# Kernel tuning notes

Hardware: AMD Instinct MI355X
Metric: run time of the kernel (lower is better)

The kernel has to match this reference:

```python
import jax, jax.numpy as jnp
import numpy as np

B, Din, T, G = 8, 512, 1024, 128
DM, H, L, FF = 512, 8, 2, 2048
MAX_PERIOD = 10000.0


def _ln(x, s, b, eps=1e-5):
    m = x.mean(-1, keepdims=True)
    v = ((x - m) ** 2).mean(-1, keepdims=True)
    return (x - m) * jax.lax.rsqrt(v + eps) * s + b


def _rope(x, pos):
    # x: (B,H,S,Dh), pos: (S,)
    dh = x.shape[-1]
    half = dh // 2
    freqs = 1.0 / (MAX_PERIOD ** (jnp.arange(half, dtype=jnp.float32) / half))
    ang = pos[:, None] * freqs[None, :]              # (S, half)
    cos, sin = jnp.cos(ang), jnp.sin(ang)
    x1, x2 = x[..., :half], x[..., half:]
    return jnp.concatenate([x1 * cos - x2 * sin, x1 * sin + x2 * cos], axis=-1)


def _transformer(x, W_in, b_in, ln1_s, ln1_b, Wq, Wk, Wv, Wo, ls1,
                 ln2_s, ln2_b, W1, b1, W2, b2, ls2, lnf_s, lnf_b, W_out, b_out):
    # x: (B, Din, S) conv layout -> (B, S, DM)
    h = jnp.einsum('bds,de->bse', x, W_in) + b_in
    Bx, S, E = h.shape
    dh = E // H
    pos = jnp.arange(S, dtype=jnp.float32)
    scale = 1.0 / jnp.sqrt(jnp.asarray(dh, h.dtype))
    for l in range(Wq.shape[0]):
        y = _ln(h, ln1_s[l], ln1_b[l])
        q = (y @ Wq[l]).reshape(Bx, S, H, dh).transpose(0, 2, 1, 3)
        k = (y @ Wk[l]).reshape(Bx, S, H, dh).transpose(0, 2, 1, 3)
        v = (y @ Wv[l]).reshape(Bx, S, H, dh).transpose(0, 2, 1, 3)
        q, k = _rope(q, pos), _rope(k, pos)
        att = jax.nn.softmax(jnp.einsum('bhqd,bhkd->bhqk', q, k) * scale, axis=-1)
        o = jnp.einsum('bhqk,bhkd->bhqd', att, v).transpose(0, 2, 1, 3).reshape(Bx, S, E)
        h = h + ls1[l] * (o @ Wo[l])
        y = _ln(h, ln2_s[l], ln2_b[l])
        h = h + ls2[l] * (jax.nn.gelu(y @ W1[l] + b1[l]) @ W2[l] + b2[l])
    h = _ln(h, lnf_s, lnf_b)
    return (h @ W_out + b_out).transpose(0, 2, 1)  # (B, Din, S)


def _forward(features, alignment_matrix, num_segments_per_item, params):
    Bx, D, Tt = features.shape
    Gx = alignment_matrix.shape[1]
    ar_t = jnp.arange(Tt, dtype=jnp.int32)
    ar_g = jnp.arange(Gx, dtype=jnp.int32)
    group_mask = ar_g[None, :] < num_segments_per_item[:, None]          # (B,G)
    group_last = (alignment_matrix * ar_t.astype(features.dtype)).max(axis=2).astype(jnp.int32)  # (B,G)
    valid_last = jnp.where(group_mask, group_last, -1)
    frame_lengths = valid_last.max(axis=1) + 1                            # (B,)
    frame_mask = ar_t[None, :] < frame_lengths[:, None]                   # (B,T)
    last_for_count = jnp.where(group_mask, group_last, Tt + 1)
    num_q_before = jnp.sum(last_for_count[:, :, None] < ar_t[None, None, :], axis=1).astype(jnp.int32)  # (B,T)
    frame_dest = ar_t[None, :] + num_q_before                             # (B,T)
    query_dest = group_last + ar_g[None, :] + 1                           # (B,G)
    # mean-pooled query init
    summed = jnp.einsum('bgt,bdt->bgd', alignment_matrix, features)
    counts = jnp.maximum(alignment_matrix.sum(axis=2), 1.0)
    queries = (summed / counts[..., None]).transpose(0, 2, 1)             # (B,D,G)
    source_seq = jnp.concatenate([features, queries], axis=2)             # (B,D,T+G)
    dest = jnp.concatenate([frame_dest, query_dest], axis=1)              # (B,T+G)
    smask = jnp.concatenate([frame_mask, group_mask], axis=1)
    dest_m = jnp.where(smask, dest, Tt + Gx)
    perm = jnp.argsort(dest_m, axis=1)                                    # (B,T+G)
    interleaved = jnp.take_along_axis(source_seq, perm[:, None, :], axis=2)
    tout = _transformer(interleaved, *params)                             # (B,D,T+G)
    inv_perm = jnp.argsort(perm, axis=1)
    qpos = inv_perm[:, Tt:]                                               # (B,G)
    agg = jnp.take_along_axis(tout, qpos[:, None, :], axis=2)             # (B,D,G)
    return jnp.where(group_mask[:, None, :], agg, 0.0)


def setup_inputs() -> dict:
    key = jax.random.key(0)
    ks = jax.random.split(key, 8)
    rng = np.random.default_rng(0)
    align = np.zeros((B, G, T), np.float32)
    num_seg = np.zeros((B,), np.int32)
    for b in range(B):
        n = int(rng.integers(G // 2, G + 1))
        cuts = np.sort(rng.choice(np.arange(1, T), n - 1, replace=False))
        gid = np.searchsorted(cuts, np.arange(T), side='right')
        align[b, gid, np.arange(T)] = 1.0
        num_seg[b] = n
    s = 0.02
    return {
        'features': jax.random.normal(ks[0], (B, Din, T), jnp.float32),
        'alignment_matrix': jnp.asarray(align),
        'num_segments_per_item': jnp.asarray(num_seg),
        'W_in': jax.random.normal(ks[1], (Din, DM), jnp.float32) * s,
        'b_in': jnp.zeros((DM,), jnp.float32),
        'ln1_s': jnp.ones((L, DM), jnp.float32), 'ln1_b': jnp.zeros((L, DM), jnp.float32),
        'Wq': jax.random.normal(ks[2], (L, DM, DM), jnp.float32) * s,
        'Wk': jax.random.normal(ks[3], (L, DM, DM), jnp.float32) * s,
        'Wv': jax.random.normal(ks[4], (L, DM, DM), jnp.float32) * s,
        'Wo': jax.random.normal(ks[5], (L, DM, DM), jnp.float32) * s,
        'ls1': 0.01 * jnp.ones((L, DM), jnp.float32),
        'ln2_s': jnp.ones((L, DM), jnp.float32), 'ln2_b': jnp.zeros((L, DM), jnp.float32),
        'W1': jax.random.normal(ks[6], (L, DM, FF), jnp.float32) * s,
        'b1': jnp.zeros((L, FF), jnp.float32),
        'W2': jax.random.normal(ks[7], (L, FF, DM), jnp.float32) * s,
        'b2': jnp.zeros((L, DM), jnp.float32),
        'ls2': 0.01 * jnp.ones((L, DM), jnp.float32),
        'lnf_s': jnp.ones((DM,), jnp.float32), 'lnf_b': jnp.zeros((DM,), jnp.float32),
        'W_out': jax.random.normal(jax.random.fold_in(key, 9), (DM, Din), jnp.float32) * s,
        'b_out': jnp.zeros((Din,), jnp.float32),
    }


def reference(features, alignment_matrix, num_segments_per_item, W_in, b_in, ln1_s, ln1_b,
              Wq, Wk, Wv, Wo, ls1, ln2_s, ln2_b, W1, b1, W2, b2, ls2, lnf_s, lnf_b, W_out, b_out):
    params = (W_in, b_in, ln1_s, ln1_b, Wq, Wk, Wv, Wo, ls1,
              ln2_s, ln2_b, W1, b1, W2, b2, ls2, lnf_s, lnf_b, W_out, b_out)
    return _forward(features, alignment_matrix, num_segments_per_item, params)
```

## Files before the change

### kernel.cpp

```cpp
#include <hip/hip_runtime.h>
#include <hip/hip_bf16.h>
#include <math.h>

#define NB   8
#define NT   1024
#define NG   128
#define NS   1152
#define NDIN 512
#define NDM  512
#define NH   8
#define NDH  64
#define NFF  2048
#define NL   2

typedef __attribute__((ext_vector_type(4))) float  floatx4;
typedef __attribute__((ext_vector_type(8))) short  shortx8;

__device__ __forceinline__ float gelu_f(float x) {
    float u = 1.5957691216057308f * (x + 0.044715f * x * x * x);
    return x / (1.0f + __expf(-u));
}

__device__ __forceinline__ void gload_lds16(const void* g, void* l) {
    __builtin_amdgcn_global_load_lds((const __attribute__((address_space(1))) unsigned int*)g,
                                     (__attribute__((address_space(3))) unsigned int*)l, 16, 0, 0);
}

__device__ __forceinline__ short f2bfs(float x) {
    __hip_bfloat16 h = __float2bfloat16(x);
    return *(short*)&h;
}
__device__ __forceinline__ unsigned pack_bf2(float a, float b) {
    __hip_bfloat16 x = __float2bfloat16(a), y = __float2bfloat16(b);
    return ((unsigned)(*(unsigned short*)&y) << 16) | (*(unsigned short*)&x);
}

__global__ __launch_bounds__(256) void ropetab_k(float2* __restrict__ tab)
{
    const int idx = blockIdx.x * 256 + threadIdx.x;
    if (idx >= NS * 32) return;
    const int s = idx >> 5, i = idx & 31;
    const float fr = __expf(-(float)i * 0.28782313662425576f);
    const float ang = (float)s * fr;
    tab[idx] = make_float2(cosf(ang), sinf(ang));
}

__global__ __launch_bounds__(256) void pool_k(const float* __restrict__ align,
        const float* __restrict__ features, int* __restrict__ glast,
        float* __restrict__ queries)
{
    __shared__ float redf[256];
    __shared__ int   redi[256];
    __shared__ float aw[NT];
    const int bg = blockIdx.x;
    const int b = bg >> 7;
    const int tid = threadIdx.x;
    const float* arow = align + (size_t)bg * NT;
    float cnt = 0.f, last = 0.f;
    int tmin = NT;
    for (int t = tid; t < NT; t += 256) {
        float a = arow[t];
        cnt += a;
        last = fmaxf(last, a * (float)t);
        if (a > 0.f) tmin = min(tmin, t);
    }
    redf[tid] = cnt; __syncthreads();
    for (int s = 128; s > 0; s >>= 1) { if (tid < s) redf[tid] += redf[tid + s]; __syncthreads(); }
    float c = redf[0]; __syncthreads();
    redf[tid] = last; __syncthreads();
    for (int s = 128; s > 0; s >>= 1) { if (tid < s) redf[tid] = fmaxf(redf[tid], redf[tid + s]); __syncthreads(); }
    float l = redf[0];
    redi[tid] = tmin; __syncthreads();
    for (int s = 128; s > 0; s >>= 1) { if (tid < s) redi[tid] = min(redi[tid], redi[tid + s]); __syncthreads(); }
    const int t0 = redi[0];
    const int t1 = (int)l;
    if (tid == 0) glast[bg] = t1;
    __syncthreads();
    for (int t = t0 + tid; t <= t1; t += 256) aw[t - t0] = arow[t];
    __syncthreads();
    const float invc = 1.0f / fmaxf(c, 1.0f);
    for (int d = tid; d < NDIN; d += 256) {
        const float* frow = features + ((size_t)b * NDIN + d) * NT;
        float s = 0.f;
        for (int t = t0; t <= t1; ++t) s += aw[t - t0] * frow[t];
        queries[(size_t)bg * NDIN + d] = s * invc;
    }
}

__global__ __launch_bounds__(256) void rank_k(const int* __restrict__ glast,
        const int* __restrict__ nsegp, int* __restrict__ perm, int* __restrict__ qpos)
{
    __shared__ int dm[NS];
    __shared__ int gl[NG];
    const int b = blockIdx.y;
    const int tid = threadIdx.x;
    const int j = blockIdx.x * 256 + tid;
    if (tid < NG) gl[tid] = glast[b * NG + tid];
    const int ns = nsegp[b];
    __syncthreads();
    for (int jj = tid; jj < NS; jj += 256) {
        int d;
        if (jj < NT) {
            int t = jj, nq = 0, flen = 0;
            for (int g = 0; g < ns; ++g) {
                flen = max(flen, gl[g] + 1);
                nq += (gl[g] < t) ? 1 : 0;
            }
            d = (t < flen) ? (t + nq) : NS;
        } else {
            int g = jj - NT;
            d = (g < ns) ? (gl[g] + g + 1) : NS;
        }
        dm[jj] = d;
    }
    __syncthreads();
    if (j < NS) {
        const int my = dm[j];
        int r = 0;
        for (int t = 0; t < NS; ++t) {
            int v2 = dm[t];
            r += (v2 < my || (v2 == my && t < j)) ? 1 : 0;
        }
        perm[b * NS + r] = j;
        if (j >= NT) qpos[b * NG + (j - NT)] = r;
    }
}

__global__ __launch_bounds__(256) void buildx_k(const float* __restrict__ features,
        const float* __restrict__ queries, const int* __restrict__ perm,
        __hip_bfloat16* __restrict__ X)
{
    const int idx = blockIdx.x * 256 + threadIdx.x;
    if (idx >= NB * NS * NDIN) return;
    const int d = idx & (NDIN - 1);
    const int p = (idx >> 9) % NS;
    const int b = idx / (NS * NDIN);
    const int j = perm[b * NS + p];
    float v = (j < NT) ? features[((size_t)b * NDIN + d) * NT + j]
                       : queries[((size_t)(b * NG + (j - NT))) * NDIN + d];
    X[idx] = __float2bfloat16(v);
}

__device__ __forceinline__ void wtile(const float* __restrict__ src,
        __hip_bfloat16* __restrict__ dst, int K, int N, int i, int tid, short tile[32][33])
{
    const int gx = N / 32;
    const int n0 = (i % gx) * 32;
    const int k0 = (i / gx) * 32;
    {
        const int r = tid >> 3, c4 = (tid & 7) * 4;
        float4 v = *(const float4*)&src[(size_t)(k0 + r) * N + n0 + c4];
        tile[c4 + 0][r] = f2bfs(v.x);
        tile[c4 + 1][r] = f2bfs(v.y);
        tile[c4 + 2][r] = f2bfs(v.z);
        tile[c4 + 3][r] = f2bfs(v.w);
    }
    __syncthreads();
    {
        const int r = tid >> 3, c4 = (tid & 7) * 4;
        short* dp = (short*)dst + (size_t)(n0 + r) * K + k0 + c4;
        short4 v;
        v.x = tile[r][c4 + 0]; v.y = tile[r][c4 + 1];
        v.z = tile[r][c4 + 2]; v.w = tile[r][c4 + 3];
        *(short4*)dp = v;
    }
}

__global__ __launch_bounds__(256) void wtransall_k(
        const float* W_in, const float* Wq, const float* Wk, const float* Wv,
        const float* Wo, const float* W1, const float* W2, const float* W_out,
        __hip_bfloat16* w_inT, __hip_bfloat16* wqkvT0, __hip_bfloat16* wqkvT1,
        __hip_bfloat16* woT0, __hip_bfloat16* woT1,
        __hip_bfloat16* w1T0, __hip_bfloat16* w1T1,
        __hip_bfloat16* w2T0, __hip_bfloat16* w2T1, __hip_bfloat16* woutT)
{
    __shared__ short tile[32][33];
    const int tid = threadIdx.x;
    const int i = blockIdx.x;
    const float* src; __hip_bfloat16* dst; int K, N, ti;
    if (i < 256) { src = W_in; dst = w_inT; K = 512; N = 512; ti = i; }
    else if (i < 6400) {
        int r = i - 256;
        const int l = r / 3072; r -= l * 3072;
        const size_t o5 = (size_t)l * 262144, o2 = (size_t)l * 1048576;
        if (r < 256)       { src = Wq + o5; dst = (l ? wqkvT1 : wqkvT0);          K = 512;  N = 512;  ti = r; }
        else if (r < 512)  { src = Wk + o5; dst = (l ? wqkvT1 : wqkvT0) + 262144; K = 512;  N = 512;  ti = r - 256; }
        else if (r < 768)  { src = Wv + o5; dst = (l ? wqkvT1 : wqkvT0) + 524288; K = 512;  N = 512;  ti = r - 512; }
        else if (r < 1024) { src = Wo + o5; dst = (l ? woT1 : woT0);              K = 512;  N = 512;  ti = r - 768; }
        else if (r < 2048) { src = W1 + o2; dst = (l ? w1T1 : w1T0);              K = 512;  N = 2048; ti = r - 1024; }
        else               { src = W2 + o2; dst = (l ? w2T1 : w2T0);              K = 2048; N = 512;  ti = r - 2048; }
    }
    else { src = W_out; dst = woutT; K = 512; N = 512; ti = i - 6400; }
    wtile(src, dst, K, N, ti, tid, tile);
}

__global__ __launch_bounds__(256) void bgemmw1_k(const __hip_bfloat16* __restrict__ A,
        const __hip_bfloat16* __restrict__ Bt, __hip_bfloat16* __restrict__ Cout,
        const float* __restrict__ bias, int M, int N, int K)
{
    __shared__ __align__(16) short SM[4][128 * 32];
    short* As0 = SM[0]; short* As1 = SM[1];
    short* Bs0 = SM[2]; short* Bs1 = SM[3];
    const int tid = threadIdx.x;
    const int wave = tid >> 6, lane = tid & 63;
    const int quad = lane >> 4, l16 = lane & 15;
    const int wm = wave >> 1, wn = wave & 1;
    const size_t bm = (size_t)blockIdx.y * 128, bn = (size_t)blockIdx.x * 128;
    const int sw = (l16 >> 1) & 3;
    const short* Ag = (const short*)A;
    const short* Bg = (const short*)Bt;
    const int lrow = lane >> 2;
    const int lchunk = (lane & 3) ^ ((lane >> 3) & 3);

    floatx4 acc[4][4];
#pragma unroll
    for (int i = 0; i < 4; ++i)
#pragma unroll
        for (int j = 0; j < 4; ++j) acc[i][j] = (floatx4){0.f, 0.f, 0.f, 0.f};

    for (int k0 = 0; k0 < K; k0 += 64) {
        __syncthreads();
#pragma unroll
        for (int c = 0; c < 2; ++c) {
            const int r0 = (c * 4 + wave) * 16;
            const size_t ra = (bm + r0 + lrow) * (size_t)K + k0 + lchunk * 8;
            const size_t rb = (bn + r0 + lrow) * (size_t)K + k0 + lchunk * 8;
            gload_lds16(Ag + ra,      &As0[r0 * 32]);
            gload_lds16(Ag + ra + 32, &As1[r0 * 32]);
            gload_lds16(Bg + rb,      &Bs0[r0 * 32]);
            gload_lds16(Bg + rb + 32, &Bs1[r0 * 32]);
        }
        __syncthreads();
#pragma unroll
        for (int h = 0; h < 2; ++h) {
            const short* Asrc = h ? As1 : As0;
            const short* Bsrc = h ? Bs1 : Bs0;
            shortx8 af[4], bf[4];
#pragma unroll
            for (int t = 0; t < 4; ++t) {
                af[t] = *(const shortx8*)&Asrc[(wm * 64 + t * 16 + l16) * 32 + ((quad ^ sw) * 8)];
                bf[t] = *(const shortx8*)&Bsrc[(wn * 64 + t * 16 + l16) * 32 + ((quad ^ sw) * 8)];
            }
#pragma unroll
            for (int mt = 0; mt < 4; ++mt)
#pragma unroll
                for (int nt = 0; nt < 4; ++nt)
                    acc[mt][nt] = __builtin_amdgcn_mfma_f32_16x16x32_bf16(af[mt], bf[nt], acc[mt][nt], 0, 0, 0);
        }
    }
    __syncthreads();
    const size_t mbase = bm + wm * 64;
    const size_t nbase = bn + wn * 64;
    short* ep = &SM[wave][0];
#pragma unroll
    for (int nt = 0; nt < 4; ++nt) {
        const size_t n = nbase + nt * 16 + l16;
        const float bz = bias[n];
        const int col = nt * 16 + l16;
#pragma unroll
        for (int mt = 0; mt < 4; ++mt)
#pragma unroll
            for (int r = 0; r < 4; ++r) {
                const int rl = mt * 16 + quad * 4 + r;
                float e = gelu_f(acc[mt][nt][r] + bz);
                ep[rl * 64 + (((col >> 3) ^ (rl & 7)) * 8) + (col & 7)] = f2bfs(e);
            }
    }
    __asm__ __volatile__("" ::: "memory");
#pragma unroll
    for (int c2 = 0; c2 < 8; ++c2) {
        const int rl = c2 * 8 + (lane >> 3);
        const int cc = lane & 7;
        shortx8 v = *(const shortx8*)&ep[rl * 64 + ((cc ^ (rl & 7)) * 8)];
        *(shortx8*)((short*)Cout + (mbase + rl) * N + nbase + cc * 8) = v;
    }
}

__global__ __launch_bounds__(256) void bgemmqkv_k(const __hip_bfloat16* __restrict__ A,
        const __hip_bfloat16* __restrict__ Bt, __hip_bfloat16* __restrict__ qh,
        __hip_bfloat16* __restrict__ kh, __hip_bfloat16* __restrict__ vT,
        const float2* __restrict__ tab)
{
    __shared__ __align__(16) short SM[4][128 * 32];
    short* As0 = SM[0]; short* As1 = SM[1];
    short* Bs0 = SM[2]; short* Bs1 = SM[3];
    const int tid = threadIdx.x;
    const int wave = tid >> 6, lane = tid & 63;
    const int quad = lane >> 4, l16 = lane & 15;
    const int wm = wave >> 1, wn = wave & 1;
    const size_t bm = (size_t)blockIdx.y * 128, bn = (size_t)blockIdx.x * 128;
    const int sw = (l16 >> 1) & 3;
    const int K = 512;
    const short* Ag = (const short*)A;
    const short* Bg = (const short*)Bt;
    const int lrow = lane >> 2;
    const int lchunk = (lane & 3) ^ ((lane >> 3) & 3);

    floatx4 acc[4][4];
#pragma unroll
    for (int i = 0; i < 4; ++i)
#pragma unroll
        for (int j = 0; j < 4; ++j) acc[i][j] = (floatx4){0.f, 0.f, 0.f, 0.f};

    for (int k0 = 0; k0 < K; k0 += 64) {
        __syncthreads();
#pragma unroll
        for (int c = 0; c < 2; ++c) {
            const int r0 = (c * 4 + wave) * 16;
            const size_t ra = (bm + r0 + lrow) * (size_t)K + k0 + lchunk * 8;
            const size_t rb = (bn + r0 + lrow) * (size_t)K + k0 + lchunk * 8;
            gload_lds16(Ag + ra,      &As0[r0 * 32]);
            gload_lds16(Ag + ra + 32, &As1[r0 * 32]);
            gload_lds16(Bg + rb,      &Bs0[r0 * 32]);
            gload_lds16(Bg + rb + 32, &Bs1[r0 * 32]);
        }
        __syncthreads();
#pragma unroll
        for (int h = 0; h < 2; ++h) {
            const short* Asrc = h ? As1 : As0;
            const short* Bsrc = h ? Bs1 : Bs0;
            shortx8 af[4], bf[4];
#pragma unroll
            for (int t = 0; t < 4; ++t) {
                af[t] = *(const shortx8*)&Asrc[(wm * 64 + t * 16 + l16) * 32 + ((quad ^ sw) * 8)];
                bf[t] = *(const shortx8*)&Bsrc[(wn * 64 + t * 16 + l16) * 32 + ((quad ^ sw) * 8)];
            }
#pragma unroll
            for (int mt = 0; mt < 4; ++mt)
#pragma unroll
                for (int nt = 0; nt < 4; ++nt)
                    acc[mt][nt] = __builtin_amdgcn_mfma_f32_16x16x32_bf16(af[mt], bf[nt], acc[mt][nt], 0, 0, 0);
        }
    }
    __syncthreads();
    short* ep = &SM[wave][0];
    const int bidx = (int)(bm / NS);
    const int sbase = (int)(bm - (size_t)bidx * NS) + wm * 64;
    const int region = (int)(bn >> 9);
    if (region < 2) {
        const float qsc = region ? 1.0f : 0.18033688011112043f;
        const int h = (int)((((int)bn & 511) + wn * 64) >> 6);
#pragma unroll
        for (int nt = 0; nt < 2; ++nt) {
            const int d1 = nt * 16 + l16, d2 = d1 + 32;
            const float2* tp = tab + d1;
#pragma unroll
            for (int mt = 0; mt < 4; ++mt)
#pragma unroll
                for (int r = 0; r < 4; ++r) {
                    const int sl = mt * 16 + quad * 4 + r;
                    const int s = sbase + sl;
                    float x1 = acc[mt][nt][r], x2 = acc[mt][nt + 2][r];
                    float2 cs = tp[s * 32];
                    ep[sl * 64 + (((d1 >> 3) ^ (sl & 7)) * 8) + (d1 & 7)] = f2bfs(qsc * (x1 * cs.x - x2 * cs.y));
                    ep[sl * 64 + (((d2 >> 3) ^ (sl & 7)) * 8) + (d2 & 7)] = f2bfs(qsc * (x1 * cs.y + x2 * cs.x));
                }
        }
        __asm__ __volatile__("" ::: "memory");
        short* dst = (short*)(region ? kh : qh) + ((size_t)(bidx * NH + h)) * NS * NDH;
#pragma unroll
        for (int c2 = 0; c2 < 8; ++c2) {
            const int sl = c2 * 8 + (lane >> 3);
            const int cc = lane & 7;
            shortx8 v = *(const shortx8*)&ep[sl * 64 + ((cc ^ (sl & 7)) * 8)];
            *(shortx8*)(dst + (size_t)(sbase + sl) * NDH + cc * 8) = v;
        }
    } else {
        const int base = (int)(bn - 1024) + wn * 64;
        const int h = base >> 6;
#pragma unroll
        for (int nt = 0; nt < 4; ++nt) {
            const int dl = nt * 16 + l16;
#pragma unroll
            for (int mt = 0; mt < 4; ++mt)
#pragma unroll
                for (int r = 0; r < 4; ++r) {
                    const int sl = mt * 16 + quad * 4 + r;
                    ep[dl * 64 + (((sl >> 3) ^ (dl & 7)) * 8) + (sl & 7)] = f2bfs(acc[mt][nt][r]);
                }
        }
        __asm__ __volatile__("" ::: "memory");
        short* vp = (short*)vT + ((size_t)(bidx * NH + h)) * NDH * NS;
#pragma unroll
        for (int c2 = 0; c2 < 8; ++c2) {
            const int dl = c2 * 8 + (lane >> 3);
            const int cc = lane & 7;
            shortx8 v = *(const shortx8*)&ep[dl * 64 + ((cc ^ (dl & 7)) * 8)];
            *(shortx8*)(vp + (size_t)dl * NS + sbase + cc * 8) = v;
        }
    }
}

template <int EPI>
__global__ __launch_bounds__(256) void bgemm64_k(const __hip_bfloat16* __restrict__ A,
        const __hip_bfloat16* __restrict__ Bt, void* __restrict__ Cout,
        const float* __restrict__ bias, const float* __restrict__ ls,
        const float* __restrict__ res, const int* __restrict__ nsegp, int M, int N, int K)
{
    __shared__ __align__(16) short As0[64 * 32], As1[64 * 32];
    __shared__ __align__(16) short Bs0[128 * 32], Bs1[128 * 32];
    const int tid = threadIdx.x;
    const int wave = tid >> 6, lane = tid & 63;
    const int quad = lane >> 4, l16 = lane & 15;
    const int wm = wave >> 1, wn = wave & 1;
    const size_t bm = (size_t)blockIdx.y * 64, bn = (size_t)blockIdx.x * 128;
    const int sw = (l16 >> 1) & 3;
    const short* Ag = (const short*)A;
    const short* Bg = (const short*)Bt;
    const int lrow = lane >> 2;
    const int lchunk = (lane & 3) ^ ((lane >> 3) & 3);

    floatx4 acc[2][4];
#pragma unroll
    for (int i = 0; i < 2; ++i)
#pragma unroll
        for (int j = 0; j < 4; ++j) acc[i][j] = (floatx4){0.f, 0.f, 0.f, 0.f};

    for (int k0 = 0; k0 < K; k0 += 64) {
        __syncthreads();
        {
            const int rA = wave * 16;
            const size_t ra = (bm + rA + lrow) * (size_t)K + k0 + lchunk * 8;
            gload_lds16(Ag + ra,      &As0[rA * 32]);
            gload_lds16(Ag + ra + 32, &As1[rA * 32]);
            const int rB = wave * 32;
            const size_t rb0 = (bn + rB + lrow) * (size_t)K + k0 + lchunk * 8;
            const size_t rb1 = (bn + rB + 16 + lrow) * (size_t)K + k0 + lchunk * 8;
            gload_lds16(Bg + rb0,      &Bs0[rB * 32]);
            gload_lds16(Bg + rb1,      &Bs0[(rB + 16) * 32]);
            gload_lds16(Bg + rb0 + 32, &Bs1[rB * 32]);
            gload_lds16(Bg + rb1 + 32, &Bs1[(rB + 16) * 32]);
        }
        __syncthreads();
#pragma unroll
        for (int h = 0; h < 2; ++h) {
            const short* Asrc = h ? As1 : As0;
            const short* Bsrc = h ? Bs1 : Bs0;
            shortx8 af[2], bf[4];
#pragma unroll
            for (int t = 0; t < 2; ++t)
                af[t] = *(const shortx8*)&Asrc[(wm * 32 + t * 16 + l16) * 32 + ((quad ^ sw) * 8)];
#pragma unroll
            for (int t = 0; t < 4; ++t)
                bf[t] = *(const shortx8*)&Bsrc[(wn * 64 + t * 16 + l16) * 32 + ((quad ^ sw) * 8)];
#pragma unroll
            for (int mt = 0; mt < 2; ++mt)
#pragma unroll
                for (int nt = 0; nt < 4; ++nt)
                    acc[mt][nt] = __builtin_amdgcn_mfma_f32_16x16x32_bf16(af[mt], bf[nt], acc[mt][nt], 0, 0, 0);
        }
    }
    const size_t mbase = bm + wm * 32;
    const size_t nbase = bn + wn * 64;
#pragma unroll
    for (int nt = 0; nt < 4; ++nt) {
        const size_t n = nbase + nt * 16 + l16;
        const float bz = bias ? bias[n] : 0.f;
        const float lz = (EPI == 2) ? ls[n] : 0.f;
#pragma unroll
        for (int mt = 0; mt < 2; ++mt) {
#pragma unroll
            for (int r = 0; r < 4; ++r) {
                const size_t m = mbase + mt * 16 + quad * 4 + r;
                float e = acc[mt][nt][r] + bz;
                if (EPI == 4) {
                    const int b = (int)(m >> 7), g = (int)(m & 127);
                    float val = (g < nsegp[b]) ? e : 0.0f;
                    ((float*)Cout)[(size_t)b * (NDIN * NG) + n * NG + g] = val;
                } else {
                    const size_t off = m * N + n;
                    if (EPI == 2) e = res[off] + lz * e;
                    ((float*)Cout)[off] = e;
                }
            }
        }
    }
}

__global__ __launch_bounds__(256) void lnw_k(const float* __restrict__ in,
        __hip_bfloat16* __restrict__ out, const float* __restrict__ gam, const float* __restrict__ bet)
{
    const int r = blockIdx.x * 4 + (threadIdx.x >> 6);
    const int t = threadIdx.x & 63;
    const float4* xp = (const float4*)(in + (size_t)r * NDM);
    float4 a = xp[t * 2], b4 = xp[t * 2 + 1];
    float s = a.x + a.y + a.z + a.w + b4.x + b4.y + b4.z + b4.w;
#pragma unroll
    for (int o = 1; o < 64; o <<= 1) s += __shfl_xor(s, o);
    const float mean = s * (1.0f / NDM);
    float dx[8] = {a.x - mean, a.y - mean, a.z - mean, a.w - mean,
                   b4.x - mean, b4.y - mean, b4.z - mean, b4.w - mean};
    float v = 0.f;
#pragma unroll
    for (int i = 0; i < 8; ++i) v += dx[i] * dx[i];
#pragma unroll
    for (int o = 1; o < 64; o <<= 1) v += __shfl_xor(v, o);
    const float inv = rsqrtf(v * (1.0f / NDM) + 1e-5f);
    const float4* gp = (const float4*)gam;
    const float4* bp = (const float4*)bet;
    float4 g0 = gp[t * 2], g1 = gp[t * 2 + 1], q0 = bp[t * 2], q1 = bp[t * 2 + 1];
    shortx8 o8;
    o8[0] = f2bfs(dx[0] * inv * g0.x + q0.x);
    o8[1] = f2bfs(dx[1] * inv * g0.y + q0.y);
    o8[2] = f2bfs(dx[2] * inv * g0.z + q0.z);
    o8[3] = f2bfs(dx[3] * inv * g0.w + q0.w);
    o8[4] = f2bfs(dx[4] * inv * g1.x + q1.x);
    o8[5] = f2bfs(dx[5] * inv * g1.y + q1.y);
    o8[6] = f2bfs(dx[6] * inv * g1.z + q1.z);
    o8[7] = f2bfs(dx[7] * inv * g1.w + q1.w);
    *(shortx8*)((short*)out + (size_t)r * NDM + t * 8) = o8;
}

__global__ __launch_bounds__(64) void lnwg_k(const float* __restrict__ h,
        __hip_bfloat16* __restrict__ out, const float* __restrict__ gam, const float* __restrict__ bet,
        const int* __restrict__ qpos)
{
    const int r = blockIdx.x, t = threadIdx.x;
    const int b = r >> 7;
    const int src = qpos[r];
    const float4* xp = (const float4*)(h + ((size_t)(b * NS + src)) * NDM);
    float4 a = xp[t * 2], b4 = xp[t * 2 + 1];
    float s = a.x + a.y + a.z + a.w + b4.x + b4.y + b4.z + b4.w;
#pragma unroll
    for (int o = 1; o < 64; o <<= 1) s += __shfl_xor(s, o);
    const float mean = s * (1.0f / NDM);
    float dx[8] = {a.x - mean, a.y - mean, a.z - mean, a.w - mean,
                   b4.x - mean, b4.y - mean, b4.z - mean, b4.w - mean};
    float v = 0.f;
#pragma unroll
    for (int i = 0; i < 8; ++i) v += dx[i] * dx[i];
#pragma unroll
    for (int o = 1; o < 64; o <<= 1) v += __shfl_xor(v, o);
    const float inv = rsqrtf(v * (1.0f / NDM) + 1e-5f);
    const float4* gp = (const float4*)gam;
    const float4* bp = (const float4*)bet;
    float4 g0 = gp[t * 2], g1 = gp[t * 2 + 1], q0 = bp[t * 2], q1 = bp[t * 2 + 1];
    shortx8 o8;
    o8[0] = f2bfs(dx[0] * inv * g0.x + q0.x);
    o8[1] = f2bfs(dx[1] * inv * g0.y + q0.y);
    o8[2] = f2bfs(dx[2] * inv * g0.z + q0.z);
    o8[3] = f2bfs(dx[3] * inv * g0.w + q0.w);
    o8[4] = f2bfs(dx[4] * inv * g1.x + q1.x);
    o8[5] = f2bfs(dx[5] * inv * g1.y + q1.y);
    o8[6] = f2bfs(dx[6] * inv * g1.z + q1.z);
    o8[7] = f2bfs(dx[7] * inv * g1.w + q1.w);
    *(shortx8*)((short*)out + (size_t)r * NDM + t * 8) = o8;
}

#define FKT 64
#define FKP 68
#define NTL (NS / FKT)
__global__ __launch_bounds__(256) void fattn_k(const __hip_bfloat16* __restrict__ qb,
        const __hip_bfloat16* __restrict__ kb, const __hip_bfloat16* __restrict__ vbT,
        __hip_bfloat16* __restrict__ o)
{
    __shared__ __align__(16) short Ks[FKT * FKP];
    __shared__ __align__(16) short Vt[NDH * FKP];
    __shared__ __align__(16) short Pl[64 * FKP];
    const int tid = threadIdx.x;
    const int wave = tid >> 6, lane = tid & 63;
    const int quad = lane >> 4, l16 = lane & 15;
    const int L = blockIdx.x;
    const int xcd = L & 7, sl = L >> 3;
    const int bh = (xcd << 3) | (sl & 7);
    const int q0 = (sl >> 3) * 64;
    const int bb = bh >> 3, hh = bh & 7;
    const short* qbase = (const short*)qb + (size_t)bh * NS * NDH;
    const short* kbase = (const short*)kb + (size_t)bh * NS * NDH;
    const short* vbase = (const short*)vbT + (size_t)bh * NDH * NS;

    shortx8 Qf0, Qf1;
    {
        const short* qp = qbase + (size_t)(q0 + wave * 16 + l16) * NDH + quad * 8;
        Qf0 = *(const shortx8*)qp;
        Qf1 = *(const shortx8*)(qp + 32);
    }
    floatx4 Oacc[4];
#pragma unroll
    for (int i = 0; i < 4; ++i) Oacc[i] = (floatx4){0.f, 0.f, 0.f, 0.f};
    float l_s = 0.f;

    const int sr = tid >> 2, sc = (tid & 3) * 16;
    const int prow = wave * 16 + l16;
    const short* kg = kbase + (size_t)sr * NDH + sc;
    const short* vg = vbase + (size_t)sr * NS + sc;
    shortx8 pk0 = *(const shortx8*)kg, pk1 = *(const shortx8*)(kg + 8);
    shortx8 pv0 = *(const shortx8*)vg, pv1 = *(const shortx8*)(vg + 8);

    for (int t = 0; t < NTL; ++t) {
        __syncthreads();
        *(shortx8*)&Ks[sr * FKP + sc]     = pk0;
        *(shortx8*)&Ks[sr * FKP + sc + 8] = pk1;
        *(shortx8*)&Vt[sr * FKP + sc]     = pv0;
        *(shortx8*)&Vt[sr * FKP + sc + 8] = pv1;
        __syncthreads();
        if (t + 1 < NTL) {
            kg += FKT * NDH; vg += FKT;
            pk0 = *(const shortx8*)kg; pk1 = *(const shortx8*)(kg + 8);
            pv0 = *(const shortx8*)vg; pv1 = *(const shortx8*)(vg + 8);
        }

        floatx4 S[4];
#pragma unroll
        for (int kbk = 0; kbk < 4; ++kbk) {
            shortx8 kf0 = *(const shortx8*)&Ks[(kbk * 16 + l16) * FKP + quad * 8];
            shortx8 kf1 = *(const shortx8*)&Ks[(kbk * 16 + l16) * FKP + 32 + quad * 8];
            floatx4 sa = (floatx4){0.f, 0.f, 0.f, 0.f};
            sa = __builtin_amdgcn_mfma_f32_16x16x32_bf16(kf0, Qf0, sa, 0, 0, 0);
            sa = __builtin_amdgcn_mfma_f32_16x16x32_bf16(kf1, Qf1, sa, 0, 0, 0);
            S[kbk] = sa;
        }
        float e[16];
        float rs = 0.f;
#pragma unroll
        for (int kbk = 0; kbk < 4; ++kbk)
#pragma unroll
            for (int i = 0; i < 4; ++i) {
                float ee = exp2f(S[kbk][i]);
                e[kbk * 4 + i] = ee;
                rs += ee;
            }
        rs += __shfl_xor(rs, 16);
        rs += __shfl_xor(rs, 32);
        l_s += rs;
#pragma unroll
        for (int kbk = 0; kbk < 4; ++kbk) {
            uint2 u;
            u.x = pack_bf2(e[kbk * 4 + 0], e[kbk * 4 + 1]);
            u.y = pack_bf2(e[kbk * 4 + 2], e[kbk * 4 + 3]);
            *(uint2*)&Pl[prow * FKP + kbk * 16 + quad * 4] = u;
        }
        __asm__ __volatile__("" ::: "memory");
        shortx8 Pf0 = *(const shortx8*)&Pl[prow * FKP + quad * 8];
        shortx8 Pf1 = *(const shortx8*)&Pl[prow * FKP + 32 + quad * 8];
#pragma unroll
        for (int ct = 0; ct < 4; ++ct) {
            shortx8 vf0 = *(const shortx8*)&Vt[(ct * 16 + l16) * FKP + quad * 8];
            shortx8 vf1 = *(const shortx8*)&Vt[(ct * 16 + l16) * FKP + 32 + quad * 8];
            Oacc[ct] = __builtin_amdgcn_mfma_f32_16x16x32_bf16(Pf0, vf0, Oacc[ct], 0, 0, 0);
            Oacc[ct] = __builtin_amdgcn_mfma_f32_16x16x32_bf16(Pf1, vf1, Oacc[ct], 0, 0, 0);
        }
    }
    float lr[4];
#pragma unroll
    for (int i = 0; i < 4; ++i) lr[i] = __shfl(l_s, quad * 4 + i);
#pragma unroll
    for (int i = 0; i < 4; ++i) {
        const float inv = 1.0f / lr[i];
        const int row = q0 + wave * 16 + quad * 4 + i;
        __hip_bfloat16* op = o + ((size_t)(bb * NS + row)) * NDM + hh * NDH + l16;
        op[0]  = __float2bfloat16(Oacc[0][i] * inv);
        op[16] = __float2bfloat16(Oacc[1][i] * inv);
        op[32] = __float2bfloat16(Oacc[2][i] * inv);
        op[48] = __float2bfloat16(Oacc[3][i] * inv);
    }
}

extern "C" void kernel_launch(void* const* d_in, const int* in_sizes, int n_in,
                              void* d_out, int out_size, void* d_ws, size_t ws_size,
                              hipStream_t stream) {
    const float* features = (const float*)d_in[0];
    const float* align    = (const float*)d_in[1];
    const int*   nseg     = (const int*)d_in[2];
    const float* W_in  = (const float*)d_in[3];
    const float* b_in  = (const float*)d_in[4];
    const float* ln1_s = (const float*)d_in[5];
    const float* ln1_b = (const float*)d_in[6];
    const float* Wq = (const float*)d_in[7];
    const float* Wk = (const float*)d_in[8];
    const float* Wv = (const float*)d_in[9];
    const float* Wo = (const float*)d_in[10];
    const float* ls1   = (const float*)d_in[11];
    const float* ln2_s = (const float*)d_in[12];
    const float* ln2_b = (const float*)d_in[13];
    const float* W1 = (const float*)d_in[14];
    const float* b1 = (const float*)d_in[15];
    const float* W2 = (const float*)d_in[16];
    const float* b2 = (const float*)d_in[17];
    const float* ls2   = (const float*)d_in[18];
    const float* lnf_s = (const float*)d_in[19];
    const float* lnf_b = (const float*)d_in[20];
    const float* W_out = (const float*)d_in[21];
    const float* b_out = (const float*)d_in[22];

    const size_t SZ_BSD = (size_t)NB * NS * NDM;

    float* p = (float*)d_ws;
    __hip_bfloat16* w_inT  = (__hip_bfloat16*)p;
    __hip_bfloat16* wqkvT0 = w_inT + 512 * 512;
    __hip_bfloat16* wqkvT1 = wqkvT0 + 1536 * 512;
    __hip_bfloat16* woT0   = wqkvT1 + 1536 * 512;
    __hip_bfloat16* woT1   = woT0 + 512 * 512;
    __hip_bfloat16* w1T0   = woT1 + 512 * 512;
    __hip_bfloat16* w1T1   = w1T0 + 2048 * 512;
    __hip_bfloat16* w2T0   = w1T1 + 2048 * 512;
    __hip_bfloat16* w2T1   = w2T0 + 512 * 2048;
    __hip_bfloat16* woutT  = w2T1 + 512 * 2048;
    int* glast = (int*)(woutT + 512 * 512);
    int* perm  = glast + NB * NG;
    int* qpos  = perm + NB * NS;
    float2* ropetab = (float2*)(qpos + NB * NG);
    p = (float*)(ropetab + NS * 32);

    float* hbuf = p; p += SZ_BSD;
    __hip_bfloat16* ybuf = (__hip_bfloat16*)p;  p += SZ_BSD / 2;
    __hip_bfloat16* obuf = (__hip_bfloat16*)p;  p += SZ_BSD / 2;
    __hip_bfloat16* ubuf = (__hip_bfloat16*)p;  p += SZ_BSD * 2;
    __hip_bfloat16* xin  = (__hip_bfloat16*)p;  p += SZ_BSD / 2;
    float* quer = p; p += (size_t)NB * NG * NDIN;
    __hip_bfloat16* hq = (__hip_bfloat16*)p; p += (size_t)NB * NG * NDM / 2;
    const size_t needed = (size_t)((char*)p - (char*)d_ws);
    if (ws_size < needed) return;

    __hip_bfloat16* qh = ubuf;
    __hip_bfloat16* kh = ubuf + SZ_BSD;
    __hip_bfloat16* vT = xin;

    ropetab_k<<<(NS * 32 + 255) / 256, 256, 0, stream>>>(ropetab);
    wtransall_k<<<6656, 256, 0, stream>>>(W_in, Wq, Wk, Wv, Wo, W1, W2, W_out,
            w_inT, wqkvT0, wqkvT1, woT0, woT1, w1T0, w1T1, w2T0, w2T1, woutT);
    pool_k<<<NB * NG, 256, 0, stream>>>(align, features, glast, quer);
    rank_k<<<dim3((NS + 255) / 256, NB), 256, 0, stream>>>(glast, nseg, perm, qpos);
    buildx_k<<<(NB * NS * NDIN + 255) / 256, 256, 0, stream>>>(features, quer, perm, xin);

    const int M = NB * NS;
    bgemm64_k<0><<<dim3(NDM / 128, M / 64), 256, 0, stream>>>(xin, w_inT, hbuf, b_in, nullptr, nullptr, nullptr, M, NDM, NDIN);

    for (int l = 0; l < NL; ++l) {
        __hip_bfloat16* wqkvT = (l ? wqkvT1 : wqkvT0);
        __hip_bfloat16* woT   = (l ? woT1 : woT0);
        __hip_bfloat16* w1T   = (l ? w1T1 : w1T0);
        __hip_bfloat16* w2T   = (l ? w2T1 : w2T0);

        lnw_k<<<M / 4, 256, 0, stream>>>(hbuf, ybuf, ln1_s + l * NDM, ln1_b + l * NDM);
        bgemmqkv_k<<<dim3(1536 / 128, M / 128), 256, 0, stream>>>(ybuf, wqkvT, qh, kh, vT, ropetab);
        fattn_k<<<(NS / 64) * NH * NB, 256, 0, stream>>>(qh, kh, vT, obuf);
        bgemm64_k<2><<<dim3(NDM / 128, M / 64), 256, 0, stream>>>(obuf, woT, hbuf, nullptr, ls1 + l * NDM, hbuf, nullptr, M, NDM, NDM);
        lnw_k<<<M / 4, 256, 0, stream>>>(hbuf, ybuf, ln2_s + l * NDM, ln2_b + l * NDM);
        bgemmw1_k<<<dim3(NFF / 128, M / 128), 256, 0, stream>>>(ybuf, w1T, ubuf, b1 + l * NFF, M, NFF, NDM);
        bgemm64_k<2><<<dim3(NDM / 128, M / 64), 256, 0, stream>>>(ubuf, w2T, hbuf, b2 + l * NDM, ls2 + l * NDM, hbuf, nullptr, M, NDM, NFF);
    }

    lnwg_k<<<NB * NG, 64, 0, stream>>>(hbuf, hq, lnf_s, lnf_b, qpos);
    bgemm64_k<4><<<dim3(NDIN / 128, (NB * NG) / 64), 256, 0, stream>>>(hq, woutT, d_out, b_out, nullptr, nullptr, nseg, NB * NG, NDIN, NDM);
}
```

Baseline: 635.4 us.

## Transpose features once for coalesced pooling/gather; compute softmax row sums via MFMA

Adds a kernel that transposes features to (B,T,Din) so pooling and the input-gather kernel read contiguous rows, and buildx now writes four bf16 values per thread using float4 loads. In flash attention, the per-row exp sum is no longer computed with scalar adds and shuffles. Instead a ones-column fragment is multiplied with the probability tile through extra MFMAs, so the sum is taken from the same bf16-rounded P that feeds PV. The cost is an extra transpose pass over features plus a workspace buffer, and two extra MFMAs per key tile.

Result: no change. 625.0 us (-1.6%).

```diff
diff --git a/kernel.cpp b/kernel.cpp
--- a/kernel.cpp
+++ b/kernel.cpp
@@ -45,8 +45,30 @@
     tab[idx] = make_float2(cosf(ang), sinf(ang));
 }
 
+__global__ __launch_bounds__(256) void ftrans_k(const float* __restrict__ f, float* __restrict__ ft)
+{
+    __shared__ float tile[32][33];
+    const int tid = threadIdx.x;
+    const int t0 = blockIdx.x * 32;
+    const int d0 = blockIdx.y * 32;
+    const int b  = blockIdx.z;
+    const int r = tid >> 3, c4 = (tid & 7) * 4;
+    {
+        float4 v = *(const float4*)&f[((size_t)(b * NDIN + d0 + r)) * NT + t0 + c4];
+        tile[c4 + 0][r] = v.x; tile[c4 + 1][r] = v.y;
+        tile[c4 + 2][r] = v.z; tile[c4 + 3][r] = v.w;
+    }
+    __syncthreads();
+    {
+        float4 v;
+        v.x = tile[r][c4 + 0]; v.y = tile[r][c4 + 1];
+        v.z = tile[r][c4 + 2]; v.w = tile[r][c4 + 3];
+        *(float4*)&ft[((size_t)(b * NT + t0 + r)) * NDIN + d0 + c4] = v;
+    }
+}
+
 __global__ __launch_bounds__(256) void pool_k(const float* __restrict__ align,
-        const float* __restrict__ features, int* __restrict__ glast,
+        const float* __restrict__ featT, int* __restrict__ glast,
         float* __restrict__ queries)
 {
     __shared__ float redf[256];
@@ -79,10 +101,10 @@
     for (int t = t0 + tid; t <= t1; t += 256) aw[t - t0] = arow[t];
     __syncthreads();
     const float invc = 1.0f / fmaxf(c, 1.0f);
+    const float* fT = featT + (size_t)b * NT * NDIN;
     for (int d = tid; d < NDIN; d += 256) {
-        const float* frow = features + ((size_t)b * NDIN + d) * NT;
         float s = 0.f;
-        for (int t = t0; t <= t1; ++t) s += aw[t - t0] * frow[t];
+        for (int t = t0; t <= t1; ++t) s += aw[t - t0] * fT[(size_t)t * NDIN + d];
         queries[(size_t)bg * NDIN + d] = s * invc;
     }
 }
@@ -126,19 +148,23 @@
     }
 }
 
-__global__ __launch_bounds__(256) void buildx_k(const float* __restrict__ features,
+__global__ __launch_bounds__(256) void buildx_k(const float* __restrict__ featT,
         const float* __restrict__ queries, const int* __restrict__ perm,
         __hip_bfloat16* __restrict__ X)
 {
     const int idx = blockIdx.x * 256 + threadIdx.x;
-    if (idx >= NB * NS * NDIN) return;
-    const int d = idx & (NDIN - 1);
-    const int p = (idx >> 9) % NS;
-    const int b = idx / (NS * NDIN);
+    if (idx >= NB * NS * (NDIN / 4)) return;
+    const int dq = idx & 127;
+    const int p = (idx >> 7) % NS;
+    const int b = idx / (NS * 128);
     const int j = perm[b * NS + p];
-    float v = (j < NT) ? features[((size_t)b * NDIN + d) * NT + j]
-                       : queries[((size_t)(b * NG + (j - NT))) * NDIN + d];
-    X[idx] = __float2bfloat16(v);
+    const float4* src = (j < NT)
+        ? (const float4*)&featT[((size_t)(b * NT + j)) * NDIN]
+        : (const float4*)&queries[((size_t)(b * NG + (j - NT))) * NDIN];
+    float4 v = src[dq];
+    short4 o;
+    o.x = f2bfs(v.x); o.y = f2bfs(v.y); o.z = f2bfs(v.z); o.w = f2bfs(v.w);
+    *(short4*)((short*)X + ((size_t)(b * NS + p)) * NDIN + dq * 4) = o;
 }
 
 __device__ __forceinline__ void wtile(const float* __restrict__ src,
@@ -555,7 +581,7 @@
         __hip_bfloat16* __restrict__ o)
 {
     __shared__ __align__(16) short Ks[FKT * FKP];
-    __shared__ __align__(16) short Vt[NDH * FKP];
+    __shared__ __align__(16) short Vt[(NDH + 16) * FKP];
     __shared__ __align__(16) short Pl[64 * FKP];
     const int tid = threadIdx.x;
     const int wave = tid >> 6, lane = tid & 63;
@@ -575,10 +601,20 @@
         Qf0 = *(const shortx8*)qp;
         Qf1 = *(const shortx8*)(qp + 32);
     }
+    {
+        const int rr = 64 + (tid >> 4);
+        const int cc = (tid & 15) * 4;
+        short4 ones; ones.x = 0x3F80; ones.y = 0x3F80; ones.z = 0x3F80; ones.w = 0x3F80;
+        *(short4*)&Vt[rr * FKP + cc] = ones;
+    }
+    __syncthreads();
+    shortx8 Of0 = *(const shortx8*)&Vt[(64 + l16) * FKP + quad * 8];
+    shortx8 Of1 = *(const shortx8*)&Vt[(64 + l16) * FKP + 32 + quad * 8];
+
     floatx4 Oacc[4];
 #pragma unroll
     for (int i = 0; i < 4; ++i) Oacc[i] = (floatx4){0.f, 0.f, 0.f, 0.f};
-    float l_s = 0.f;
+    floatx4 Oacc5 = (floatx4){0.f, 0.f, 0.f, 0.f};
 
     const int sr = tid >> 2, sc = (tid & 3) * 16;
     const int prow = wave * 16 + l16;
@@ -610,24 +646,11 @@
             sa = __builtin_amdgcn_mfma_f32_16x16x32_bf16(kf1, Qf1, sa, 0, 0, 0);
             S[kbk] = sa;
         }
-        float e[16];
-        float rs = 0.f;
-#pragma unroll
-        for (int kbk = 0; kbk < 4; ++kbk)
-#pragma unroll
-            for (int i = 0; i < 4; ++i) {
-                float ee = exp2f(S[kbk][i]);
-                e[kbk * 4 + i] = ee;
-                rs += ee;
-            }
-        rs += __shfl_xor(rs, 16);
-        rs += __shfl_xor(rs, 32);
-        l_s += rs;
 #pragma unroll
         for (int kbk = 0; kbk < 4; ++kbk) {
             uint2 u;
-            u.x = pack_bf2(e[kbk * 4 + 0], e[kbk * 4 + 1]);
-            u.y = pack_bf2(e[kbk * 4 + 2], e[kbk * 4 + 3]);
+            u.x = pack_bf2(exp2f(S[kbk][0]), exp2f(S[kbk][1]));
+            u.y = pack_bf2(exp2f(S[kbk][2]), exp2f(S[kbk][3]));
             *(uint2*)&Pl[prow * FKP + kbk * 16 + quad * 4] = u;
         }
         __asm__ __volatile__("" ::: "memory");
@@ -640,10 +663,12 @@
             Oacc[ct] = __builtin_amdgcn_mfma_f32_16x16x32_bf16(Pf0, vf0, Oacc[ct], 0, 0, 0);
             Oacc[ct] = __builtin_amdgcn_mfma_f32_16x16x32_bf16(Pf1, vf1, Oacc[ct], 0, 0, 0);
         }
+        Oacc5 = __builtin_amdgcn_mfma_f32_16x16x32_bf16(Pf0, Of0, Oacc5, 0, 0, 0);
+        Oacc5 = __builtin_amdgcn_mfma_f32_16x16x32_bf16(Pf1, Of1, Oacc5, 0, 0, 0);
     }
     float lr[4];
 #pragma unroll
-    for (int i = 0; i < 4; ++i) lr[i] = __shfl(l_s, quad * 4 + i);
+    for (int i = 0; i < 4; ++i) lr[i] = __shfl(Oacc5[i], quad * 16);
 #pragma unroll
     for (int i = 0; i < 4; ++i) {
         const float inv = 1.0f / lr[i];
@@ -702,6 +727,7 @@
     float2* ropetab = (float2*)(qpos + NB * NG);
     p = (float*)(ropetab + NS * 32);
 
+    float* featT = p; p += (size_t)NB * NT * NDIN;
     float* hbuf = p; p += SZ_BSD;
     __hip_bfloat16* ybuf = (__hip_bfloat16*)p;  p += SZ_BSD / 2;
     __hip_bfloat16* obuf = (__hip_bfloat16*)p;  p += SZ_BSD / 2;
@@ -717,11 +743,12 @@
     __hip_bfloat16* vT = xin;
 
     ropetab_k<<<(NS * 32 + 255) / 256, 256, 0, stream>>>(ropetab);
+    ftrans_k<<<dim3(NT / 32, NDIN / 32, NB), 256, 0, stream>>>(features, featT);
     wtransall_k<<<6656, 256, 0, stream>>>(W_in, Wq, Wk, Wv, Wo, W1, W2, W_out,
             w_inT, wqkvT0, wqkvT1, woT0, woT1, w1T0, w1T1, w2T0, w2T1, woutT);
-    pool_k<<<NB * NG, 256, 0, stream>>>(align, features, glast, quer);
+    pool_k<<<NB * NG, 256, 0, stream>>>(align, featT, glast, quer);
     rank_k<<<dim3((NS + 255) / 256, NB), 256, 0, stream>>>(glast, nseg, perm, qpos);
-    buildx_k<<<(NB * NS * NDIN + 255) / 256, 256, 0, stream>>>(features, quer, perm, xin);
+    buildx_k<<<(NB * NS * (NDIN / 4) + 255) / 256, 256, 0, stream>>>(featT, quer, perm, xin);
 
     const int M = NB * NS;
     bgemm64_k<0><<<dim3(NDM / 128, M / 64), 256, 0, stream>>>(xin, w_inT, hbuf, b_in, nullptr, nullptr, nullptr, M, NDM, NDIN);
```
